# Performance work log

Measured on AMD Instinct MI355X. Metric: run time of the kernel, lower is better.

## Reference

```python
import jax, jax.numpy as jnp
import numpy as np

ALPHA, GAMMA = 0.25, 2.0
CLASS_W, COORD_W, MASK_W = 2.0, 5.0, 5.0
EPS = 1e-8


def point_sample(masks, coords):
    """Bilinear sample (grid_sample, align_corners=False, zero padding).
    masks: [R, H, W]; coords: [P, 2] as (x, y) in [0, 1]. Returns [R, P]."""
    H, W = masks.shape[-2:]
    gx = 2.0 * coords[:, 0] - 1.0
    gy = 2.0 * coords[:, 1] - 1.0
    x = ((gx + 1.0) * W - 1.0) * 0.5
    y = ((gy + 1.0) * H - 1.0) * 0.5
    x0 = jnp.floor(x)
    y0 = jnp.floor(y)
    wx1 = x - x0
    wy1 = y - y0
    wx0 = 1.0 - wx1
    wy0 = 1.0 - wy1
    x0i = x0.astype(jnp.int32)
    y0i = y0.astype(jnp.int32)
    x1i = x0i + 1
    y1i = y0i + 1

    def gather(ix, iy):
        valid = ((ix >= 0) & (ix < W) & (iy >= 0) & (iy < H)).astype(masks.dtype)
        ixc = jnp.clip(ix, 0, W - 1)
        iyc = jnp.clip(iy, 0, H - 1)
        return masks[:, iyc, ixc] * valid  # [R, P]

    return (gather(x0i, y0i) * (wx0 * wy0)
            + gather(x1i, y0i) * (wx1 * wy0)
            + gather(x0i, y1i) * (wx0 * wy1)
            + gather(x1i, y1i) * (wx1 * wy1))


def setup_inputs() -> dict:
    key = jax.random.key(0)
    k1, k2, k3, k4, k5, k6 = jax.random.split(key, 6)
    bs, Q, n_ctrl, Hm, Wm, T, P = 8, 300, 16, 128, 128, 160, 12544
    return {
        "pred_logits": jax.random.normal(k1, (bs, Q, 1), jnp.float32),
        "pred_ctrl_points": jax.random.uniform(k2, (bs, Q, n_ctrl, 2), jnp.float32),
        "pred_seg_mask": jax.random.normal(k3, (bs, Q, Hm, Wm), jnp.float32),
        "tgt_pts": jax.random.uniform(k4, (T, n_ctrl, 2), jnp.float32),
        "tgt_masks": jax.random.uniform(k5, (T, Hm, Wm), jnp.float32),
        "point_coords": jax.random.uniform(k6, (P, 2), jnp.float32),
        "lvl": 0,
    }


def reference(pred_logits, pred_ctrl_points, pred_seg_mask, tgt_pts, tgt_masks, point_coords, lvl):
    bs, Q = pred_logits.shape[:2]
    out_prob = jax.nn.sigmoid(pred_logits.reshape(bs * Q, -1))          # [N, 1]
    out_pts = pred_ctrl_points.reshape(bs * Q, -1)                      # [N, 2*n_ctrl]
    tgt_flat = tgt_pts.reshape(tgt_pts.shape[0], -1)                    # [T, 2*n_ctrl]

    cost_mask_dice = 0.0
    if lvl < 2:  # num_seg_layers
        out_masks = pred_seg_mask.reshape(bs * Q, *pred_seg_mask.shape[-2:])
        # nearest-interp of tgt_masks to out_masks size is identity (same size)
        t_pts_samp = point_sample(tgt_masks, point_coords)              # [T, P]
        o_pts_samp = point_sample(out_masks, point_coords)              # [N, P]
        s = jax.nn.sigmoid(o_pts_samp)                                  # dice_loss sigmoids inputs
        numerator = 2.0 * jnp.einsum('np,tp->nt', s, t_pts_samp)        # [N, T]
        denominator = s.sum(-1)[:, None] + t_pts_samp.sum(-1)[None, :]
        cost_mask_dice = 1.0 - (numerator + 1.0) / (denominator + 1.0)

    neg_cost = (1.0 - ALPHA) * out_prob ** GAMMA * (-jnp.log(1.0 - out_prob + EPS))
    pos_cost = ALPHA * (1.0 - out_prob) ** GAMMA * (-jnp.log(out_prob + EPS))
    cost_class = pos_cost - neg_cost                                    # [N, 1]

    cost_kpts = jnp.abs(out_pts[:, None, :] - tgt_flat[None, :, :]).sum(-1)  # L1 cdist [N, T]

    C = CLASS_W * cost_class + COORD_W * cost_kpts + MASK_W * cost_mask_dice
    return C.reshape(bs, Q, -1)
```

## Files before the change

### kernel.cpp

```cpp
#include <hip/hip_runtime.h>
#include <hip/hip_bf16.h>
#include <cstdint>

#define HW 128
#define MASK_ELEMS (HW * HW)
#define SBLK 1024
#define NBLK 256

typedef unsigned short ushort_t;
typedef __attribute__((ext_vector_type(4))) unsigned short ushort4_t;
typedef __attribute__((ext_vector_type(8))) short short8;
typedef __attribute__((ext_vector_type(4))) float f32x4;

__device__ __forceinline__ float asf(unsigned int u) {
    union { unsigned int i; float f; } c;
    c.i = u;
    return c.f;
}
__device__ __forceinline__ ushort_t f2bf(float f) {
    union { float f; unsigned int i; } c;
    c.f = f;
    unsigned int r = c.i + 0x7FFFu + ((c.i >> 16) & 1u);
    return (ushort_t)(r >> 16);
}
__device__ __forceinline__ unsigned pack2(float a, float b) {
    return (unsigned)f2bf(a) | ((unsigned)f2bf(b) << 16);
}

#define LDS_BARRIER()                                         \
    do {                                                      \
        asm volatile("s_waitcnt lgkmcnt(0)" ::: "memory");    \
        __builtin_amdgcn_s_barrier();                         \
    } while (0)

struct PMeta { int b; unsigned u0, u1; };
__device__ __forceinline__ PMeta prep_point(float cx, float cy) {
    float x = cx * (float)HW - 0.5f;
    float y = cy * (float)HW - 0.5f;
    float x0f = floorf(x), y0f = floorf(y);
    float wx1 = x - x0f, wy1 = y - y0f;
    float wx0 = 1.f - wx1, wy0 = 1.f - wy1;
    int x0 = (int)x0f, y0 = (int)y0f;
    float wxA = (x0 >= 0) ? wx0 : wx1;
    float wxB = (x0 >= 0 && x0 < HW - 1) ? wx1 : 0.f;
    float wyA = (y0 >= 0) ? wy0 : wy1;
    float wyB = (y0 >= 0 && y0 < HW - 1) ? wy1 : 0.f;
    int bx = max(x0, 0), by = max(y0, 0);
    if (bx > HW - 2) { bx = HW - 2; wxB = wxA; wxA = 0.f; }
    if (by > HW - 2) { by = HW - 2; wyB = wyA; wyA = 0.f; }
    PMeta m;
    m.b = by * HW + bx;
    m.u0 = pack2(wxA * wyA, wxB * wyA);
    m.u1 = pack2(wxA * wyB, wxB * wyB);
    return m;
}

__global__ __launch_bounds__(SBLK) void ksamp_all(
        const float* __restrict__ pmask, const float* __restrict__ tmasks,
        const float* __restrict__ coords,
        ushort_t* __restrict__ S, ushort_t* __restrict__ tsamp,
        float* __restrict__ ssum, float* __restrict__ tsum,
        const int* __restrict__ lvl, int N, int T, int P) {
    if (*lvl >= 2) return;
    __shared__ unsigned buf[2][MASK_ELEMS];
    __shared__ float wred[2][SBLK / 64];
    __shared__ int   tmi[256];
    __shared__ uint4 tmw[256];
    __shared__ int4  tmi4[64];
    __shared__ uint4 tma[64], tmb[64];
    const int tid = threadIdx.x;
    const int lane = tid & 63;
    const int NM = N + T;
    const int nq = P >> 2;
    const int ntail = nq - 3 * SBLK;

    int4 idr[3];
    uint4 war[3], wbr[3];
    #pragma unroll
    for (int it = 0; it < 3; ++it) {
        int q = it * SBLK + tid;
        if (q < nq) {
            float4 ca = ((const float4*)coords)[2 * q];
            float4 cb = ((const float4*)coords)[2 * q + 1];
            PMeta m0 = prep_point(ca.x, ca.y), m1 = prep_point(ca.z, ca.w);
            PMeta m2 = prep_point(cb.x, cb.y), m3 = prep_point(cb.z, cb.w);
            idr[it] = make_int4(m0.b, m1.b, m2.b, m3.b);
            war[it] = make_uint4(m0.u0, m0.u1, m1.u0, m1.u1);
            wbr[it] = make_uint4(m2.u0, m2.u1, m3.u0, m3.u1);
        } else {
            idr[it] = make_int4(0, 0, 0, 0);
            war[it] = make_uint4(0, 0, 0, 0);
            wbr[it] = make_uint4(0, 0, 0, 0);
        }
    }
    if (ntail > 0 && tid < ntail && tid < 64) {
        int q = 3 * SBLK + tid;
        float4 ca = ((const float4*)coords)[2 * q];
        float4 cb = ((const float4*)coords)[2 * q + 1];
        PMeta m0 = prep_point(ca.x, ca.y), m1 = prep_point(ca.z, ca.w);
        PMeta m2 = prep_point(cb.x, cb.y), m3 = prep_point(cb.z, cb.w);
        tmi4[tid] = make_int4(m0.b, m1.b, m2.b, m3.b);
        tma[tid] = make_uint4(m0.u0, m0.u1, m1.u0, m1.u1);
        tmb[tid] = make_uint4(m2.u0, m2.u1, m3.u0, m3.u1);
    }

    auto mptr = [&](int mi) -> const float* {
        return (mi < N) ? pmask + (size_t)mi * MASK_ELEMS
                        : tmasks + (size_t)(mi - N) * MASK_ELEMS;
    };

    const int b = blockIdx.x;
    const int rounds = (NM - b + NBLK - 1) / NBLK;
    if (rounds <= 0) return;

    float4 rS[4];
    float nxr[4];
    auto load_mask = [&](const float* g) {
        #pragma unroll
        for (int j = 0; j < 4; ++j) {
            int o = j * (SBLK * 4) + tid * 4;
            rS[j] = *(const float4*)(g + o);
            nxr[j] = (lane == 63) ? g[min(o + 4, MASK_ELEMS - 1)] : 0.f;
        }
    };
    auto pack_mask = [&](unsigned* l) {
        #pragma unroll
        for (int j = 0; j < 4; ++j) {
            int o = j * (SBLK * 4) + tid * 4;
            float4 v = rS[j];
            float nx = __shfl_down(v.x, 1);
            if (lane == 63) nx = nxr[j];
            uint4 e = make_uint4(pack2(v.x, v.y), pack2(v.y, v.z),
                                 pack2(v.z, v.w), pack2(v.w, nx));
            *(uint4*)&l[o] = e;
        }
    };

    load_mask(mptr(b));
    pack_mask(buf[0]);
    if (rounds > 1) load_mask(mptr(b + NBLK));
    LDS_BARRIER();

    int cur = 0;
    for (int k = 0; k < rounds; ++k) {
        if (k + 1 < rounds) {
            pack_mask(buf[cur ^ 1]);
            if (k + 2 < rounds) load_mask(mptr(b + (k + 2) * NBLK));
        }
        const unsigned* lm = buf[cur];
        const int mi = b + k * NBLK;
        const bool sig = (mi < N);
        ushort4_t* o4 = sig ? (ushort4_t*)(S + (size_t)mi * P)
                            : (ushort4_t*)(tsamp + (size_t)(mi - N) * P);
        float sum = 0.f;

        auto do_quad = [&](int4 id, uint4 wa4, uint4 wb4, int q) {
            float v[4];
            int bi[4] = {id.x, id.y, id.z, id.w};
            unsigned ua[4] = {wa4.x, wa4.z, wb4.x, wb4.z};
            unsigned ub[4] = {wa4.y, wa4.w, wb4.y, wb4.w};
            #pragma unroll
            for (int p2 = 0; p2 < 4; ++p2) {
                int bb = bi[p2];
                unsigned r0 = lm[bb];
                unsigned r1 = lm[bb + HW];
                float vv = asf(ua[p2] << 16) * asf(r0 << 16)
                         + asf(ua[p2] & 0xffff0000u) * asf(r0 & 0xffff0000u)
                         + asf(ub[p2] << 16) * asf(r1 << 16)
                         + asf(ub[p2] & 0xffff0000u) * asf(r1 & 0xffff0000u);
                if (sig) vv = __builtin_amdgcn_rcpf(1.f + __expf(-vv));
                v[p2] = vv;
            }
            ushort4_t o = {f2bf(v[0]), f2bf(v[1]), f2bf(v[2]), f2bf(v[3])};
            o4[q] = o;
            sum += (v[0] + v[1]) + (v[2] + v[3]);
        };

        #pragma unroll
        for (int it = 0; it < 3; ++it) {
            int q = it * SBLK + tid;
            if (q < nq) do_quad(idr[it], war[it], wbr[it], q);
        }
        if (ntail > 0 && ntail <= 64) {
            int tq = tid >> 4;
            if (((tid & 15) == 0) && tq < ntail)
                do_quad(tmi4[tq], tma[tq], tmb[tq], 3 * SBLK + tq);
        }

        #pragma unroll
        for (int m2 = 32; m2 > 0; m2 >>= 1) sum += __shfl_xor(sum, m2, 64);
        if (lane == 0) wred[k & 1][tid >> 6] = sum;
        LDS_BARRIER();
        if (tid == 0) {
            float s = 0.f;
            #pragma unroll
            for (int w2 = 0; w2 < SBLK / 64; ++w2) s += wred[k & 1][w2];
            if (sig) ssum[mi] = s;
            else tsum[mi - N] = s;
        }
        cur ^= 1;
    }
}

#define LDF(Aarr, Barr, kof)                                                              \
    do {                                                                                  \
        _Pragma("unroll") for (int m_ = 0; m_ < 3; ++m_)                                  \
            Aarr[m_] = *(const short8*)(pa + (size_t)m_ * 16 * P + (kof));                \
        _Pragma("unroll") for (int j_ = 0; j_ < 5; ++j_)                                  \
            Barr[j_] = *(const short8*)(pb + (size_t)j_ * 16 * P + (kof));                \
    } while (0)

#define FMAS(Aarr, Barr)                                                                  \
    do {                                                                                  \
        _Pragma("unroll") for (int m_ = 0; m_ < 3; ++m_) {                                \
            _Pragma("unroll") for (int j_ = 0; j_ < 5; ++j_)                              \
                acc[m_][j_] = __builtin_amdgcn_mfma_f32_16x16x32_bf16(                    \
                    Aarr[m_], Barr[j_], acc[m_][j_], 0, 0, 0);                            \
        }                                                                                 \
    } while (0)

__global__ __launch_bounds__(256) void kgemm(const ushort_t* __restrict__ S,
                                             const ushort_t* __restrict__ Tm,
                                             float* __restrict__ Cpart,
                                             const int* __restrict__ lvl,
                                             int N, int T, int P, int nsteps) {
    if (*lvl >= 2) return;
    int tid = threadIdx.x;
    int wid = tid >> 6, lane = tid & 63;
    int wm = wid >> 1, wt = wid & 1;
    int r = lane & 15, g = lane >> 4;
    int n0 = blockIdx.x * 96 + wm * 48;
    int t0 = wt * 80;
    size_t k0 = (size_t)blockIdx.y * nsteps * 32 + g * 8;
    const ushort_t* pa = S + (size_t)(n0 + r) * P + k0;
    const ushort_t* pb = Tm + (size_t)(t0 + r) * P + k0;

    f32x4 acc[3][5];
    #pragma unroll
    for (int m2 = 0; m2 < 3; ++m2)
        #pragma unroll
        for (int j2 = 0; j2 < 5; ++j2) acc[m2][j2] = (f32x4){0.f, 0.f, 0.f, 0.f};

    short8 a0[3], b0[5], a1[3], b1[5];
    LDF(a0, b0, 0);
    int ks = 0;
    for (; ks + 2 < nsteps; ks += 2) {
        LDF(a1, b1, (ks + 1) * 32);
        FMAS(a0, b0);
        LDF(a0, b0, (ks + 2) * 32);
        FMAS(a1, b1);
    }
    LDF(a1, b1, (ks + 1) * 32);
    FMAS(a0, b0);
    FMAS(a1, b1);

    size_t cb = (size_t)blockIdx.y * N * T;
    #pragma unroll
    for (int m2 = 0; m2 < 3; ++m2)
        #pragma unroll
        for (int j2 = 0; j2 < 5; ++j2)
            #pragma unroll
            for (int q = 0; q < 4; ++q) {
                int row = n0 + m2 * 16 + g * 4 + q;
                int col = t0 + j2 * 16 + r;
                Cpart[cb + (size_t)row * T + col] = acc[m2][j2][q];
            }
}

__global__ void kfinal(const float* __restrict__ logits, const float* __restrict__ opts,
                       const float* __restrict__ tpts, const float* __restrict__ Cpart,
                       const float* __restrict__ ssum, const float* __restrict__ tsum,
                       const int* __restrict__ lvl, float* __restrict__ out,
                       int N, int T, int nks) {
    int idx = blockIdx.x * 256 + threadIdx.x;
    if (idx >= N * T) return;
    int n = idx / T, t = idx - n * T;

    float lg = logits[n];
    float p = 1.f / (1.f + __expf(-lg));
    float pos = 0.25f * (1.f - p) * (1.f - p) * (-logf(p + 1e-8f));
    float neg = 0.75f * p * p * (-logf(1.f - p + 1e-8f));
    float ccls = pos - neg;

    float kp = 0.f;
    const float4* a4 = (const float4*)(opts + (size_t)n * 32);
    const float4* b4 = (const float4*)(tpts + (size_t)t * 32);
    #pragma unroll
    for (int j = 0; j < 8; ++j) {
        float4 a = a4[j], b = b4[j];
        kp += fabsf(a.x - b.x) + fabsf(a.y - b.y) + fabsf(a.z - b.z) + fabsf(a.w - b.w);
    }

    float dice = 0.f;
    if (*lvl < 2) {
        float dot = 0.f;
        for (int ks = 0; ks < nks; ++ks) dot += Cpart[(size_t)ks * N * T + idx];
        dice = 1.f - (2.f * dot + 1.f) / (ssum[n] + tsum[t] + 1.f);
    }
    out[idx] = 2.f * ccls + 5.f * kp + 5.f * dice;
}

extern "C" void kernel_launch(void* const* d_in, const int* in_sizes, int n_in,
                              void* d_out, int out_size, void* d_ws, size_t ws_size,
                              hipStream_t stream) {
    const float* logits = (const float*)d_in[0];
    const float* cpts   = (const float*)d_in[1];
    const float* pmask  = (const float*)d_in[2];
    const float* tpts   = (const float*)d_in[3];
    const float* tmasks = (const float*)d_in[4];
    const float* coords = (const float*)d_in[5];
    const int*   lvl    = (const int*)d_in[6];
    float* out = (float*)d_out;

    int N = in_sizes[0];
    int T = in_sizes[3] / 32;
    int P = in_sizes[5] / 2;

    char* w = (char*)d_ws;
    auto alloc = [&](size_t bytes) {
        char* r = w;
        w += (bytes + 255) & ~(size_t)255;
        return r;
    };
    ushort_t* tsamp = (ushort_t*)alloc((size_t)T * P * 2);
    ushort_t* S     = (ushort_t*)alloc((size_t)N * P * 2);
    float*    ssumb = (float*)alloc((size_t)N * 4);
    float*    tsumb = (float*)alloc((size_t)T * 4);
    size_t base_bytes = (size_t)(w - (char*)d_ws);

    int nks = 14;
    if (base_bytes + (size_t)nks * N * T * 4 > ws_size) nks = 7;
    int nsteps = (P / 32) / nks;
    float* Cpart = (float*)alloc((size_t)nks * N * T * 4);

    ksamp_all<<<NBLK, SBLK, 0, stream>>>(pmask, tmasks, coords, S, tsamp,
                                         ssumb, tsumb, lvl, N, T, P);
    kgemm<<<dim3(N / 96, nks), 256, 0, stream>>>(S, tsamp, Cpart, lvl, N, T, P, nsteps);
    kfinal<<<(N * T + 255) / 256, 256, 0, stream>>>(logits, cpts, tpts, Cpart, ssumb, tsumb,
                                                    lvl, out, N, T, nks);
}
```

Before: 120.2 us.

## Drop LDS double buffering in mask sampler and double the block count

The point-sampling kernel now uses a single 64 KB LDS mask buffer instead of two, and loads, converts and stores each mask inside the round loop, followed by a barrier. The register prefetch of the next mask is gone. The grid doubles from 256 to 512 blocks so each block handles half as many masks. The goal is to fit two blocks per CU and hide memory latency through occupancy rather than software pipelining, at the cost of an extra barrier and exposed global-load latency in each round.

```diff
diff --git a/kernel.cpp b/kernel.cpp
--- a/kernel.cpp
+++ b/kernel.cpp
@@ -5,7 +5,7 @@
 #define HW 128
 #define MASK_ELEMS (HW * HW)
 #define SBLK 1024
-#define NBLK 256
+#define NBLK 512
 
 typedef unsigned short ushort_t;
 typedef __attribute__((ext_vector_type(4))) unsigned short ushort4_t;
@@ -62,10 +62,8 @@
         float* __restrict__ ssum, float* __restrict__ tsum,
         const int* __restrict__ lvl, int N, int T, int P) {
     if (*lvl >= 2) return;
-    __shared__ unsigned buf[2][MASK_ELEMS];
+    __shared__ unsigned buf[MASK_ELEMS];
     __shared__ float wred[2][SBLK / 64];
-    __shared__ int   tmi[256];
-    __shared__ uint4 tmw[256];
     __shared__ int4  tmi4[64];
     __shared__ uint4 tma[64], tmb[64];
     const int tid = threadIdx.x;
@@ -113,42 +111,27 @@
     const int rounds = (NM - b + NBLK - 1) / NBLK;
     if (rounds <= 0) return;
 
-    float4 rS[4];
-    float nxr[4];
-    auto load_mask = [&](const float* g) {
-        #pragma unroll
-        for (int j = 0; j < 4; ++j) {
-            int o = j * (SBLK * 4) + tid * 4;
-            rS[j] = *(const float4*)(g + o);
-            nxr[j] = (lane == 63) ? g[min(o + 4, MASK_ELEMS - 1)] : 0.f;
-        }
-    };
-    auto pack_mask = [&](unsigned* l) {
-        #pragma unroll
-        for (int j = 0; j < 4; ++j) {
-            int o = j * (SBLK * 4) + tid * 4;
-            float4 v = rS[j];
-            float nx = __shfl_down(v.x, 1);
-            if (lane == 63) nx = nxr[j];
-            uint4 e = make_uint4(pack2(v.x, v.y), pack2(v.y, v.z),
-                                 pack2(v.z, v.w), pack2(v.w, nx));
-            *(uint4*)&l[o] = e;
-        }
-    };
-
-    load_mask(mptr(b));
-    pack_mask(buf[0]);
-    if (rounds > 1) load_mask(mptr(b + NBLK));
-    LDS_BARRIER();
-
-    int cur = 0;
     for (int k = 0; k < rounds; ++k) {
-        if (k + 1 < rounds) {
-            pack_mask(buf[cur ^ 1]);
-            if (k + 2 < rounds) load_mask(mptr(b + (k + 2) * NBLK));
-        }
-        const unsigned* lm = buf[cur];
         const int mi = b + k * NBLK;
+        {
+            const float* g = mptr(mi);
+            #pragma unroll
+            for (int j = 0; j < 4; ++j) {
+                int o = j * (SBLK * 4) + tid * 4;
+                float4 v = *(const float4*)(g + o);
+                float nx;
+                {
+                    nx = __shfl_down(v.x, 1);
+                    if (lane == 63) nx = g[min(o + 4, MASK_ELEMS - 1)];
+                }
+                uint4 e = make_uint4(pack2(v.x, v.y), pack2(v.y, v.z),
+                                     pack2(v.z, v.w), pack2(v.w, nx));
+                *(uint4*)&buf[o] = e;
+            }
+        }
+        LDS_BARRIER();
+
+        const unsigned* lm = buf;
         const bool sig = (mi < N);
         ushort4_t* o4 = sig ? (ushort4_t*)(S + (size_t)mi * P)
                             : (ushort4_t*)(tsamp + (size_t)(mi - N) * P);
@@ -198,7 +181,6 @@
             if (sig) ssum[mi] = s;
             else tsum[mi - N] = s;
         }
-        cur ^= 1;
     }
 }
 
```

New measurement: 135.1 us. 1.12x slower.
